# Performance work log

Hardware: AMD Instinct MI355X
Metric: run time of the kernel (lower is better)

Reference implementation:

```python
import jax, jax.numpy as jnp
import numpy as np
from jax.ops import segment_sum, segment_max

N_NODES = 100000
N_EDGES = 1600000
IN, HID, OUT = 256, 64, 40
NEG_SLOPE = 0.2  # DGL GATConv default


def setup_inputs() -> dict:
    key = jax.random.key(0)
    ks = jax.random.split(key, 12)
    feat = jax.random.normal(ks[0], (N_NODES, IN), dtype=jnp.float32)
    src = jax.random.randint(ks[1], (N_EDGES,), 0, N_NODES)
    dst = jax.random.randint(ks[2], (N_EDGES,), 0, N_NODES)
    def xavier(k, shape):
        fan = sum(shape)
        return jax.random.normal(k, shape, dtype=jnp.float32) * jnp.sqrt(2.0 / fan)
    return {
        "feat": feat, "src": src, "dst": dst,
        "W1": xavier(ks[3], (IN, HID)),  "b1": jnp.zeros((HID,), jnp.float32),
        "al1": xavier(ks[4], (HID,)),    "ar1": xavier(ks[5], (HID,)),
        "W2": xavier(ks[6], (HID, OUT)), "b2": jnp.zeros((OUT,), jnp.float32),
        "al2": xavier(ks[7], (OUT,)),    "ar2": xavier(ks[8], (OUT,)),
    }


def gat_layer(x, W, b, attn_l, attn_r, src, dst, n):
    # z: [N, F_out] projected features
    z = x @ W
    el = z @ attn_l          # [N] source attention logits
    er = z @ attn_r          # [N] destination attention logits
    e = jax.nn.leaky_relu(el[src] + er[dst], NEG_SLOPE)  # [E]
    # segment (per-destination) softmax over incoming edges
    m = segment_max(e, dst, num_segments=n)              # [N]
    w = jnp.exp(e - m[dst])                              # [E]
    s = segment_sum(w, dst, num_segments=n)              # [N]
    alpha = w / s[dst]                                   # [E]
    # scatter-add aggregation of alpha * z[src]
    out = segment_sum(alpha[:, None] * z[src], dst, num_segments=n)
    return out + b


def reference(feat, src, dst, W1, b1, al1, ar1, W2, b2, al2, ar2):
    n = feat.shape[0]
    h = gat_layer(feat, W1, b1, al1, ar1, src, dst, n)
    h = jax.nn.relu(h)  # dropout is identity in eval mode
    h = gat_layer(h, W2, b2, al2, ar2, src, dst, n)
    return jax.nn.log_softmax(h, axis=-1)  # [N, out_size]
```

## Files before the change

### kernel.cpp

```cpp
#include <hip/hip_runtime.h>
#include <math.h>

constexpr int NN   = 100000;
constexpr int NE   = 1600000;
constexpr int FIN  = 256;
constexpr int HID  = 64;
constexpr int FOUT = 40;
constexpr float SLOPE = 0.2f;
constexpr int NB    = (NN + 255) / 256;
constexpr int NBUCK = NB;
constexpr int TILE_A = 8192;
constexpr int NWG_A = (NE + TILE_A - 1) / TILE_A;

__global__ __launch_bounds__(256) void gemm1_kernel(
    const float* __restrict__ feat, const float* __restrict__ W1,
    const float* __restrict__ al, const float* __restrict__ ar,
    const int* __restrict__ dst, int* __restrict__ deg,
    float* __restrict__ z, float* __restrict__ el, float* __restrict__ er)
{
    {
        int base = (blockIdx.x * 256 + threadIdx.x) * 4;
        if (base < NE) {
            const int4 d4 = *(const int4*)&dst[base];
            atomicAdd(&deg[d4.x], 1); atomicAdd(&deg[d4.y], 1);
            atomicAdd(&deg[d4.z], 1); atomicAdd(&deg[d4.w], 1);
        }
    }

    __shared__ float sT[64 * 65];
    __shared__ float sB[64 * 64];
    const int t  = threadIdx.x;
    const int tm = t >> 4;
    const int tc = t & 15;
    const int ntile = blockIdx.x * 64;

    float acc[4][4] = {};

    for (int kt = 0; kt < 4; ++kt) {
        #pragma unroll
        for (int i = 0; i < 4; ++i) {
            int nloc = tm + 16 * i;
            int n = ntile + nloc; if (n >= NN) n = NN - 1;
            float4 f = *(const float4*)&feat[(size_t)n * FIN + kt * 64 + tc * 4];
            int kk = tc * 4;
            sT[(kk + 0) * 65 + nloc] = f.x;
            sT[(kk + 1) * 65 + nloc] = f.y;
            sT[(kk + 2) * 65 + nloc] = f.z;
            sT[(kk + 3) * 65 + nloc] = f.w;
        }
        #pragma unroll
        for (int i = 0; i < 4; ++i) {
            int vec = t + 256 * i;
            *(float4*)&sB[vec * 4] = *(const float4*)&W1[kt * 4096 + vec * 4];
        }
        __syncthreads();
        #pragma unroll 8
        for (int k = 0; k < 64; ++k) {
            float a0 = sT[k * 65 + 4 * tm + 0];
            float a1 = sT[k * 65 + 4 * tm + 1];
            float a2 = sT[k * 65 + 4 * tm + 2];
            float a3 = sT[k * 65 + 4 * tm + 3];
            float4 b = *(const float4*)&sB[k * 64 + 4 * tc];
            acc[0][0] += a0 * b.x; acc[0][1] += a0 * b.y; acc[0][2] += a0 * b.z; acc[0][3] += a0 * b.w;
            acc[1][0] += a1 * b.x; acc[1][1] += a1 * b.y; acc[1][2] += a1 * b.z; acc[1][3] += a1 * b.w;
            acc[2][0] += a2 * b.x; acc[2][1] += a2 * b.y; acc[2][2] += a2 * b.z; acc[2][3] += a2 * b.w;
            acc[3][0] += a3 * b.x; acc[3][1] += a3 * b.y; acc[3][2] += a3 * b.z; acc[3][3] += a3 * b.w;
        }
        __syncthreads();
    }

    float alv[4], arv[4];
    #pragma unroll
    for (int j = 0; j < 4; ++j) { alv[j] = al[4 * tc + j]; arv[j] = ar[4 * tc + j]; }

    #pragma unroll
    for (int i = 0; i < 4; ++i) {
        int n = ntile + 4 * tm + i;
        float pl = acc[i][0] * alv[0] + acc[i][1] * alv[1] + acc[i][2] * alv[2] + acc[i][3] * alv[3];
        float pr = acc[i][0] * arv[0] + acc[i][1] * arv[1] + acc[i][2] * arv[2] + acc[i][3] * arv[3];
        #pragma unroll
        for (int off = 8; off >= 1; off >>= 1) {
            pl += __shfl_xor(pl, off);
            pr += __shfl_xor(pr, off);
        }
        if (n < NN) {
            float4 zv = make_float4(acc[i][0], acc[i][1], acc[i][2], acc[i][3]);
            *(float4*)&z[(size_t)n * HID + 4 * tc] = zv;
            if (tc == 0) { el[n] = pl; er[n] = pr; }
        }
    }
}

__global__ __launch_bounds__(256) void gemm2_kernel(
    const float* __restrict__ h, const float* __restrict__ W2,
    const float* __restrict__ al, const float* __restrict__ ar,
    float* __restrict__ z2, float* __restrict__ el, float* __restrict__ er)
{
    __shared__ float sh[4][64];
    const int w = threadIdx.x >> 6, lane = threadIdx.x & 63;
    const int n = blockIdx.x * 4 + w;
    sh[w][lane] = h[(size_t)n * HID + lane];
    __syncthreads();
    float acc = 0.f;
    if (lane < FOUT) {
        #pragma unroll 8
        for (int k = 0; k < 64; ++k) acc += sh[w][k] * W2[k * FOUT + lane];
    }
    float pl = (lane < FOUT) ? acc * al[lane] : 0.f;
    float pr = (lane < FOUT) ? acc * ar[lane] : 0.f;
    #pragma unroll
    for (int off = 32; off >= 1; off >>= 1) { pl += __shfl_xor(pl, off); pr += __shfl_xor(pr, off); }
    if (lane == 0) { el[n] = pl; er[n] = pr; }
    if (lane < FOUT) z2[(size_t)n * FOUT + lane] = acc;
}

__global__ __launch_bounds__(256) void scan_reduce_kernel(
    const int* __restrict__ deg, int* __restrict__ bsum)
{
    __shared__ int tmp[256];
    int idx = blockIdx.x * 256 + threadIdx.x;
    int v = (idx < NN) ? deg[idx] : 0;
    tmp[threadIdx.x] = v; __syncthreads();
    for (int off = 128; off >= 1; off >>= 1) {
        if (threadIdx.x < off) tmp[threadIdx.x] += tmp[threadIdx.x + off];
        __syncthreads();
    }
    if (threadIdx.x == 0) bsum[blockIdx.x] = tmp[0];
}

__global__ __launch_bounds__(512) void scan_top_kernel(
    const int* __restrict__ bsum, int* __restrict__ bofs, int* __restrict__ row_ptr)
{
    __shared__ int tmp[512];
    int t = threadIdx.x;
    int v = (t < NB) ? bsum[t] : 0;
    tmp[t] = v; __syncthreads();
    for (int off = 1; off < 512; off <<= 1) {
        int x = (t >= off) ? tmp[t - off] : 0;
        __syncthreads();
        tmp[t] += x;
        __syncthreads();
    }
    int excl = tmp[t] - v;
    if (t < NB) bofs[t] = excl;
    if (t == NB - 1) row_ptr[NN] = excl + v;
}

__global__ __launch_bounds__(256) void scan_final_kernel(
    const int* __restrict__ deg, const int* __restrict__ bofs,
    int* __restrict__ row_ptr, int* __restrict__ gcur)
{
    __shared__ int tmp[256];
    int t = threadIdx.x;
    int idx = blockIdx.x * 256 + t;
    int v = (idx < NN) ? deg[idx] : 0;
    tmp[t] = v; __syncthreads();
    for (int off = 1; off < 256; off <<= 1) {
        int x = (t >= off) ? tmp[t - off] : 0;
        __syncthreads();
        tmp[t] += x;
        __syncthreads();
    }
    if (idx < NN) row_ptr[idx] = bofs[blockIdx.x] + tmp[t] - v;
    if (t == 0) gcur[blockIdx.x] = bofs[blockIdx.x];
}

__global__ __launch_bounds__(256) void partitionA_kernel(
    const int* __restrict__ src, const int* __restrict__ dst,
    int* __restrict__ gcur, int* __restrict__ ebuck)
{
    __shared__ int hist[NBUCK];
    __shared__ int lcur[NBUCK];
    const int t = threadIdx.x;
    const int e0 = blockIdx.x * TILE_A;
    const int e1 = (e0 + TILE_A < NE) ? e0 + TILE_A : NE;

    for (int i = t; i < NBUCK; i += 256) hist[i] = 0;
    __syncthreads();
    for (int e = e0 + t; e < e1; e += 256)
        atomicAdd(&hist[dst[e] >> 8], 1);
    __syncthreads();
    for (int i = t; i < NBUCK; i += 256) {
        int hv = hist[i];
        lcur[i] = hv ? atomicAdd(&gcur[i], hv) : 0;
    }
    __syncthreads();
    for (int e = e0 + t; e < e1; e += 256) {
        int d = dst[e], s = src[e];
        int p = atomicAdd(&lcur[d >> 8], 1);
        ebuck[p] = (s << 8) | (d & 255);
    }
}

__global__ __launch_bounds__(256) void partitionB_kernel(
    const int* __restrict__ row_ptr, const int* __restrict__ ebuck,
    int* __restrict__ esrc)
{
    __shared__ int lcur[256];
    const int b = blockIdx.x;
    const int n0 = b << 8;
    const int n1 = (n0 + 256 < NN) ? n0 + 256 : NN;
    const int t = threadIdx.x;
    if (n0 + t < n1) lcur[t] = row_ptr[n0 + t];
    __syncthreads();
    const int r0 = row_ptr[n0], r1 = row_ptr[n1];
    for (int e = r0 + t; e < r1; e += 256) {
        int pk = ebuck[e];
        int p = atomicAdd(&lcur[pk & 255], 1);
        esrc[p] = pk >> 8;
    }
}

template<int F, bool FINAL_LAYER>
__global__ __launch_bounds__(256) void gat_gather_kernel(
    const int* __restrict__ row_ptr, const int* __restrict__ esrc,
    const float* __restrict__ el, const float* __restrict__ er,
    const float* __restrict__ z, const float* __restrict__ bias,
    float* __restrict__ out)
{
    __shared__ float sw[4][64];
    __shared__ int   ssn[4][64];
    const int w = threadIdx.x >> 6, lane = threadIdx.x & 63;
    const int d = blockIdx.x * 4 + w;
    const int r0 = row_ptr[d], r1 = row_ptr[d + 1];
    const int cnt = r1 - r0;
    const float erd = er[d];

    float accv = 0.f;
    float s = 0.f;

    if (cnt <= 64) {
        int sn = 0; float v = -INFINITY;
        if (lane < cnt) {
            sn = esrc[r0 + lane];
            v = el[sn] + erd;
            v = (v >= 0.f) ? v : SLOPE * v;
        }
        float m = v;
        #pragma unroll
        for (int off = 32; off >= 1; off >>= 1) m = fmaxf(m, __shfl_xor(m, off));
        float wv = (lane < cnt) ? __expf(v - m) : 0.f;
        s = wv;
        #pragma unroll
        for (int off = 32; off >= 1; off >>= 1) s += __shfl_xor(s, off);
        sw[w][lane] = wv; ssn[w][lane] = sn;
        if (lane < F) {
            int j = 0;
            for (; j + 8 <= cnt; j += 8) {
                float acc0 = 0.f, acc1 = 0.f;
                #pragma unroll
                for (int q = 0; q < 8; q += 2) {
                    float wa = sw[w][j + q],     wb = sw[w][j + q + 1];
                    int   sa = ssn[w][j + q],    sb = ssn[w][j + q + 1];
                    acc0 += wa * z[(size_t)sa * F + lane];
                    acc1 += wb * z[(size_t)sb * F + lane];
                }
                accv += acc0 + acc1;
            }
            for (; j < cnt; ++j)
                accv += sw[w][j] * z[(size_t)ssn[w][j] * F + lane];
        }
    } else {
        float m = -INFINITY;
        for (int e = r0 + lane; e < r1; e += 64) {
            float v = el[esrc[e]] + erd;
            v = (v >= 0.f) ? v : SLOPE * v;
            m = fmaxf(m, v);
        }
        #pragma unroll
        for (int off = 32; off >= 1; off >>= 1) m = fmaxf(m, __shfl_xor(m, off));
        for (int base = r0; base < r1; base += 64) {
            int e = base + lane;
            float wv = 0.f; int sn = 0;
            if (e < r1) {
                sn = esrc[e];
                float v = el[sn] + erd;
                v = (v >= 0.f) ? v : SLOPE * v;
                wv = __expf(v - m);
            }
            sw[w][lane] = wv; ssn[w][lane] = sn;
            s += wv;
            int c = r1 - base; if (c > 64) c = 64;
            if (lane < F) {
                for (int j = 0; j < c; ++j)
                    accv += sw[w][j] * z[(size_t)ssn[w][j] * F + lane];
            }
        }
        #pragma unroll
        for (int off = 32; off >= 1; off >>= 1) s += __shfl_xor(s, off);
    }

    float res = (cnt > 0) ? (accv / s) : 0.f;

    if (!FINAL_LAYER) {
        if (lane < F) {
            float v = res + bias[lane];
            out[(size_t)d * F + lane] = (v > 0.f) ? v : 0.f;
        }
    } else {
        float v = (lane < F) ? res + bias[lane] : -INFINITY;
        float mx = v;
        #pragma unroll
        for (int off = 32; off >= 1; off >>= 1) mx = fmaxf(mx, __shfl_xor(mx, off));
        float ex = (lane < F) ? __expf(v - mx) : 0.f;
        float sm = ex;
        #pragma unroll
        for (int off = 32; off >= 1; off >>= 1) sm += __shfl_xor(sm, off);
        if (lane < F) out[(size_t)d * F + lane] = v - mx - __logf(sm);
    }
}

extern "C" void kernel_launch(void* const* d_in, const int* in_sizes, int n_in,
                              void* d_out, int out_size, void* d_ws, size_t ws_size,
                              hipStream_t stream) {
    const float* feat = (const float*)d_in[0];
    const int*   src  = (const int*)d_in[1];
    const int*   dst  = (const int*)d_in[2];
    const float* W1   = (const float*)d_in[3];
    const float* b1   = (const float*)d_in[4];
    const float* al1  = (const float*)d_in[5];
    const float* ar1  = (const float*)d_in[6];
    const float* W2   = (const float*)d_in[7];
    const float* b2   = (const float*)d_in[8];
    const float* al2  = (const float*)d_in[9];
    const float* ar2  = (const float*)d_in[10];
    float* out = (float*)d_out;

    float* ws    = (float*)d_ws;
    float* z1    = ws;
    float* h     = z1 + (size_t)NN * HID;
    float* el1   = h + (size_t)NN * HID;
    float* er1   = el1 + NN;
    float* el2   = er1 + NN;
    float* er2   = el2 + NN;
    int*   deg   = (int*)(er2 + NN);
    int*   rowp  = deg + NN;
    int*   bsum  = rowp + NN + 1;
    int*   bofs  = bsum + NB;
    int*   gcur  = bofs + NB;
    int*   esrc  = gcur + NBUCK;
    int*   ebuck = (int*)h;
    float* z2    = z1;

    hipMemsetAsync(deg, 0, NN * sizeof(int), stream);

    gemm1_kernel<<<(NN + 63) / 64, 256, 0, stream>>>(feat, W1, al1, ar1, dst, deg, z1, el1, er1);

    scan_reduce_kernel<<<NB, 256, 0, stream>>>(deg, bsum);
    scan_top_kernel<<<1, 512, 0, stream>>>(bsum, bofs, rowp);
    scan_final_kernel<<<NB, 256, 0, stream>>>(deg, bofs, rowp, gcur);
    partitionA_kernel<<<NWG_A, 256, 0, stream>>>(src, dst, gcur, ebuck);
    partitionB_kernel<<<NBUCK, 256, 0, stream>>>(rowp, ebuck, esrc);

    gat_gather_kernel<HID, false><<<NN / 4, 256, 0, stream>>>(rowp, esrc, el1, er1, z1, b1, h);

    gemm2_kernel<<<NN / 4, 256, 0, stream>>>(h, W2, al2, ar2, z2, el2, er2);
    gat_gather_kernel<FOUT, true><<<NN / 4, 256, 0, stream>>>(rowp, esrc, el2, er2, z2, b2, out);
}
```

Baseline: 479.7 us.

## Use bf16 MFMA for first-layer projection GEMM with pre-transposed weights

```diff
diff --git a/kernel.cpp b/kernel.cpp
--- a/kernel.cpp
+++ b/kernel.cpp
@@ -11,9 +11,29 @@
 constexpr int NBUCK = NB;
 constexpr int TILE_A = 8192;
 constexpr int NWG_A = (NE + TILE_A - 1) / TILE_A;
+constexpr int AK = 264;
+
+typedef short  short8  __attribute__((ext_vector_type(8)));
+typedef float  floatx4 __attribute__((ext_vector_type(4)));
+
+__device__ inline unsigned short f2bf(float x) {
+    union { float f; unsigned int u; } c; c.f = x;
+    unsigned int u = c.u;
+    return (unsigned short)((u + 0x7FFF + ((u >> 16) & 1)) >> 16);
+}
+
+__global__ __launch_bounds__(256) void w1t_kernel(
+    const float* __restrict__ W1, unsigned short* __restrict__ W1T)
+{
+    int idx = blockIdx.x * 256 + threadIdx.x;
+    if (idx < FIN * HID) {
+        int k = idx >> 6, n = idx & 63;
+        W1T[n * FIN + k] = f2bf(W1[idx]);
+    }
+}
 
 __global__ __launch_bounds__(256) void gemm1_kernel(
-    const float* __restrict__ feat, const float* __restrict__ W1,
+    const float* __restrict__ feat, const unsigned short* __restrict__ W1T,
     const float* __restrict__ al, const float* __restrict__ ar,
     const int* __restrict__ dst, int* __restrict__ deg,
     float* __restrict__ z, float* __restrict__ el, float* __restrict__ er)
@@ -27,66 +47,74 @@
         }
     }
 
-    __shared__ float sT[64 * 65];
-    __shared__ float sB[64 * 64];
-    const int t  = threadIdx.x;
-    const int tm = t >> 4;
-    const int tc = t & 15;
+    __shared__ unsigned short sA[64 * AK];
+    __shared__ unsigned short sBT[64 * AK];
+    const int t = threadIdx.x;
     const int ntile = blockIdx.x * 64;
 
-    float acc[4][4] = {};
-
-    for (int kt = 0; kt < 4; ++kt) {
-        #pragma unroll
-        for (int i = 0; i < 4; ++i) {
-            int nloc = tm + 16 * i;
-            int n = ntile + nloc; if (n >= NN) n = NN - 1;
-            float4 f = *(const float4*)&feat[(size_t)n * FIN + kt * 64 + tc * 4];
-            int kk = tc * 4;
-            sT[(kk + 0) * 65 + nloc] = f.x;
-            sT[(kk + 1) * 65 + nloc] = f.y;
-            sT[(kk + 2) * 65 + nloc] = f.z;
-            sT[(kk + 3) * 65 + nloc] = f.w;
-        }
-        #pragma unroll
-        for (int i = 0; i < 4; ++i) {
-            int vec = t + 256 * i;
-            *(float4*)&sB[vec * 4] = *(const float4*)&W1[kt * 4096 + vec * 4];
-        }
-        __syncthreads();
-        #pragma unroll 8
-        for (int k = 0; k < 64; ++k) {
-            float a0 = sT[k * 65 + 4 * tm + 0];
-            float a1 = sT[k * 65 + 4 * tm + 1];
-            float a2 = sT[k * 65 + 4 * tm + 2];
-            float a3 = sT[k * 65 + 4 * tm + 3];
-            float4 b = *(const float4*)&sB[k * 64 + 4 * tc];
-            acc[0][0] += a0 * b.x; acc[0][1] += a0 * b.y; acc[0][2] += a0 * b.z; acc[0][3] += a0 * b.w;
-            acc[1][0] += a1 * b.x; acc[1][1] += a1 * b.y; acc[1][2] += a1 * b.z; acc[1][3] += a1 * b.w;
-            acc[2][0] += a2 * b.x; acc[2][1] += a2 * b.y; acc[2][2] += a2 * b.z; acc[2][3] += a2 * b.w;
-            acc[3][0] += a3 * b.x; acc[3][1] += a3 * b.y; acc[3][2] += a3 * b.z; acc[3][3] += a3 * b.w;
-        }
-        __syncthreads();
-    }
-
-    float alv[4], arv[4];
-    #pragma unroll
-    for (int j = 0; j < 4; ++j) { alv[j] = al[4 * tc + j]; arv[j] = ar[4 * tc + j]; }
-
-    #pragma unroll
-    for (int i = 0; i < 4; ++i) {
-        int n = ntile + 4 * tm + i;
-        float pl = acc[i][0] * alv[0] + acc[i][1] * alv[1] + acc[i][2] * alv[2] + acc[i][3] * alv[3];
-        float pr = acc[i][0] * arv[0] + acc[i][1] * arv[1] + acc[i][2] * arv[2] + acc[i][3] * arv[3];
+    #pragma unroll
+    for (int i = 0; i < 16; ++i) {
+        int g = t + 256 * i;
+        int row = g >> 6, kq = g & 63;
+        int n = ntile + row; if (n >= NN) n = NN - 1;
+        float4 f = *(const float4*)&feat[(size_t)n * FIN + 4 * kq];
+        ushort4 us; us.x = f2bf(f.x); us.y = f2bf(f.y); us.z = f2bf(f.z); us.w = f2bf(f.w);
+        *(ushort4*)&sA[row * AK + 4 * kq] = us;
+    }
+    #pragma unroll
+    for (int i = 0; i < 8; ++i) {
+        int g = t + 256 * i;
+        int row = g >> 5, c8 = g & 31;
+        *(uint4*)&sBT[row * AK + 8 * c8] = *(const uint4*)&W1T[row * FIN + 8 * c8];
+    }
+    __syncthreads();
+
+    const int w  = t >> 6;
+    const int l  = t & 63;
+    const int lr = l & 15;
+    const int q  = l >> 4;
+    const int m0 = 16 * w;
+
+    floatx4 acc[4];
+    #pragma unroll
+    for (int tile = 0; tile < 4; ++tile) acc[tile] = 0.f;
+
+    #pragma unroll
+    for (int kc = 0; kc < 8; ++kc) {
+        const int koff = kc * 32 + 8 * q;
+        const short8 av = *(const short8*)(sA + (m0 + lr) * AK + koff);
+        #pragma unroll
+        for (int tile = 0; tile < 4; ++tile) {
+            const short8 bv = *(const short8*)(sBT + (16 * tile + lr) * AK + koff);
+            acc[tile] = __builtin_amdgcn_mfma_f32_16x16x32_bf16(av, bv, acc[tile], 0, 0, 0);
+        }
+    }
+
+    float aln[4], arn[4];
+    #pragma unroll
+    for (int tile = 0; tile < 4; ++tile) {
+        aln[tile] = al[16 * tile + lr];
+        arn[tile] = ar[16 * tile + lr];
+    }
+    #pragma unroll
+    for (int r = 0; r < 4; ++r) {
+        int mg = ntile + m0 + 4 * q + r;
+        float pl = 0.f, pr = 0.f;
+        #pragma unroll
+        for (int tile = 0; tile < 4; ++tile) {
+            float zv = acc[tile][r];
+            pl += zv * aln[tile]; pr += zv * arn[tile];
+        }
         #pragma unroll
         for (int off = 8; off >= 1; off >>= 1) {
             pl += __shfl_xor(pl, off);
             pr += __shfl_xor(pr, off);
         }
-        if (n < NN) {
-            float4 zv = make_float4(acc[i][0], acc[i][1], acc[i][2], acc[i][3]);
-            *(float4*)&z[(size_t)n * HID + 4 * tc] = zv;
-            if (tc == 0) { el[n] = pl; er[n] = pr; }
+        if (mg < NN) {
+            #pragma unroll
+            for (int tile = 0; tile < 4; ++tile)
+                z[(size_t)mg * HID + 16 * tile + lr] = acc[tile][r];
+            if (lr == 0) { el[mg] = pl; er[mg] = pr; }
         }
     }
 }
@@ -249,9 +277,9 @@
             for (; j + 8 <= cnt; j += 8) {
                 float acc0 = 0.f, acc1 = 0.f;
                 #pragma unroll
-                for (int q = 0; q < 8; q += 2) {
-                    float wa = sw[w][j + q],     wb = sw[w][j + q + 1];
-                    int   sa = ssn[w][j + q],    sb = ssn[w][j + q + 1];
+                for (int qq = 0; qq < 8; qq += 2) {
+                    float wa = sw[w][j + qq],     wb = sw[w][j + qq + 1];
+                    int   sa = ssn[w][j + qq],    sb = ssn[w][j + qq + 1];
                     acc0 += wa * z[(size_t)sa * F + lane];
                     acc1 += wb * z[(size_t)sb * F + lane];
                 }
@@ -339,12 +367,14 @@
     int*   bofs  = bsum + NB;
     int*   gcur  = bofs + NB;
     int*   esrc  = gcur + NBUCK;
+    unsigned short* w1t = (unsigned short*)(esrc + NE);
     int*   ebuck = (int*)h;
     float* z2    = z1;
 
     hipMemsetAsync(deg, 0, NN * sizeof(int), stream);
 
-    gemm1_kernel<<<(NN + 63) / 64, 256, 0, stream>>>(feat, W1, al1, ar1, dst, deg, z1, el1, er1);
+    w1t_kernel<<<(FIN * HID + 255) / 256, 256, 0, stream>>>(W1, w1t);
+    gemm1_kernel<<<(NN + 63) / 64, 256, 0, stream>>>(feat, w1t, al1, ar1, dst, deg, z1, el1, er1);
 
     scan_reduce_kernel<<<NB, 256, 0, stream>>>(deg, bsum);
     scan_top_kernel<<<1, 512, 0, stream>>>(bsum, bofs, rowp);
```

After: 468.4 us. 1.02x faster.
